# Performance work log

Hardware: AMD Instinct MI355X
Metric: run time of the kernel (lower is better)

Reference implementation:

```python
import jax, jax.numpy as jnp
import numpy as np

K = 32
D = 256


def setup_inputs() -> dict:
    key = jax.random.key(0)
    k1, k2, kW, kV, kb = jax.random.split(key, 5)
    B, L1, L2 = 16, 256, 256
    x1 = jax.random.normal(k1, (B, L1, D), dtype=jnp.float32)
    x2 = jax.random.normal(k2, (B, L2, D), dtype=jnp.float32)
    # kaiming_uniform-style init bounds
    bound_W = np.sqrt(6.0 / ((1 + 5) * D))  # fan_in = d, a=sqrt(5)
    W = jax.random.uniform(kW, (K, D, D), minval=-bound_W, maxval=bound_W, dtype=jnp.float32)
    bound_V = np.sqrt(6.0 / ((1 + 5) * 2 * D))
    V = jax.random.uniform(kV, (K, 2 * D), minval=-bound_V, maxval=bound_V, dtype=jnp.float32)
    bound_b = 1.0 / np.sqrt(2 * D)
    b = jax.random.uniform(kb, (K,), minval=-bound_b, maxval=bound_b, dtype=jnp.float32)
    return {"x1": x1, "x2": x2, "W": W, "V": V, "b": b}


def reference(x1, x2, W, V, b):
    # x1: [B,L1,d], x2: [B,L2,d], W: [k,d,d], V: [k,2d], b: [k]
    d = x1.shape[-1]
    # bilinear term: (x1 W) x2^T per output channel k -> [B,k,L1,L2]
    temp = jnp.einsum('bld,kde->bkle', x1, W)            # [B,k,L1,d]
    bilinear_out = jnp.einsum('bkle,bme->bklm', temp, x2)  # [B,k,L1,L2]
    # linear term: V @ concat(x1,x2) = V1 x1 + V2 x2, broadcast-summed
    V1, V2 = V[:, :d], V[:, d:]
    lin1 = jnp.einsum('bld,kd->bkl', x1, V1)             # [B,k,L1]
    lin2 = jnp.einsum('bmd,kd->bkm', x2, V2)             # [B,k,L2]
    linear_out = lin1[:, :, :, None] + lin2[:, :, None, :] + b[None, :, None, None]
    return jax.nn.relu(bilinear_out + linear_out)
```

## Files before the change

### kernel.cpp

```cpp
#include <hip/hip_runtime.h>
#include <hip/hip_bf16.h>

typedef unsigned short u16;
typedef __bf16 bf16x8 __attribute__((ext_vector_type(8)));
typedef float f32x4 __attribute__((ext_vector_type(4)));

#define NB 16
#define NK 32
#define ND 256
#define NL 256

__device__ __forceinline__ u16 f2bf(float f) {
    __hip_bfloat16 h = __float2bfloat16(f);
    return __builtin_bit_cast(u16, h);
}

__device__ __forceinline__ void gload_lds16(const void* g, void* l) {
    __builtin_amdgcn_global_load_lds(
        (const __attribute__((address_space(1))) unsigned int*)g,
        (__attribute__((address_space(3))) unsigned int*)l, 16, 0, 0);
}


__global__ void prep_kernel(const float* __restrict__ x1, const float* __restrict__ x2,
                            const float* __restrict__ W,
                            u16* __restrict__ x1f, u16* __restrict__ x2f, u16* __restrict__ Wf) {
    int bid = blockIdx.x;
    int tid = threadIdx.x;
    const float* src; u16* dst; long f4;
    if (bid < 1024)      { src = x1; dst = x1f; f4 = (long)bid * 256 + tid; }
    else if (bid < 2048) { src = x2; dst = x2f; f4 = (long)(bid - 1024) * 256 + tid; }
    else                 { src = W;  dst = Wf;  f4 = (long)(bid - 2048) * 256 + tid; }
    long idx = f4 << 2;
    int mat = (int)(idx >> 16);
    int r = (int)((idx >> 8) & 255);
    int c = (int)(idx & 255);
    float4 v = ((const float4*)src)[f4];
    ushort4 o;
    o.x = f2bf(v.x); o.y = f2bf(v.y); o.z = f2bf(v.z); o.w = f2bf(v.w);
    int rt = r >> 4, ct = c >> 5;
    int lane = (r & 15) | (((c >> 3) & 3) << 4);
    long off = ((long)mat << 16) + (((rt << 3) + ct) << 9) + (lane << 3) + (c & 7);
    *(ushort4*)(dst + off) = o;
}

__launch_bounds__(512, 6)
__global__ void ntn_main(const u16* __restrict__ x1f, const u16* __restrict__ x2f,
                         const u16* __restrict__ Wf,
                         const float* __restrict__ V, const float* __restrict__ bb,
                         float* __restrict__ out) {
    __shared__ __align__(16) char ldsRaw[32768];
    __shared__ float rlin[64];

    int bid = blockIdx.x;
    int xcd   = bid & 7;
    int j     = bid >> 3;
    int slot  = j >> 7;
    int inner = j & 127;
    int st    = (slot << 3) | xcd;
    int kg = st >> 2, bg = st & 3;
    int k  = (kg << 3) | (inner >> 4);
    int b  = (bg << 2) | ((inner >> 2) & 3);
    int mq = inner & 3;

    int tid  = threadIdx.x;
    int lane = tid & 63;
    int wid  = tid >> 6;
    int lrow = lane & 15;
    int j4   = (lane >> 4) << 2;

    {
        const char* src = (const char*)(x2f + ((long)b << 16) + ((long)mq << 14));
#pragma unroll
        for (int it = 0; it < 4; ++it) {
            int chunk = (it << 3) + wid;
            gload_lds16(src + (chunk << 10) + (lane << 4), ldsRaw + (chunk << 10));
        }
    }

    float bk = bb[k];
    f32x4 acc[4][2];
    const f32x4 fz = {0.f, 0.f, 0.f, 0.f};
#pragma unroll
    for (int i = 0; i < 4; ++i) { acc[i][0] = fz; acc[i][1] = fz; }

    __syncthreads();

    {
        int ml = tid >> 3;
        int et = tid & 7;
        const float* v2p = V + ((long)k << 9) + 256 + (et << 5);
        float sum = 0.f;
#pragma unroll
        for (int eg = 0; eg < 4; ++eg) {
            int lp = (ml & 15) | (eg << 4);
            bf16x8 xv = *(const bf16x8*)(ldsRaw + ((((ml >> 4) << 3) + et) << 10) + (lp << 4));
            float4 va = *(const float4*)(v2p + (eg << 3));
            float4 vb = *(const float4*)(v2p + (eg << 3) + 4);
            sum += (float)xv[0] * va.x + (float)xv[1] * va.y + (float)xv[2] * va.z + (float)xv[3] * va.w
                 + (float)xv[4] * vb.x + (float)xv[5] * vb.y + (float)xv[6] * vb.z + (float)xv[7] * vb.w;
        }
        sum += __shfl_xor(sum, 1);
        sum += __shfl_xor(sum, 2);
        sum += __shfl_xor(sum, 4);
        if ((tid & 7) == 0) rlin[ml] = sum + bk;
    }

    {
        int wrA = wid >> 1;
        int wcA = wid & 1;
        const u16* wp = Wf + ((long)k << 16);
#pragma unroll
        for (int et = 0; et < 8; ++et) {
            bf16x8 af[4], bfr[2];
#pragma unroll
            for (int lt = 0; lt < 4; ++lt)
                af[lt] = *(const bf16x8*)(wp + (((((wrA << 2) + lt) << 3) + et) << 9) + (lane << 3));
#pragma unroll
            for (int nt = 0; nt < 2; ++nt)
                bfr[nt] = *(const bf16x8*)(ldsRaw + ((((((wcA << 1) + nt) << 3) + et) << 10) + (lane << 4)));
#pragma unroll
            for (int nt = 0; nt < 2; ++nt)
#pragma unroll
                for (int lt = 0; lt < 4; ++lt)
                    acc[lt][nt] = __builtin_amdgcn_mfma_f32_16x16x32_bf16(af[lt], bfr[nt], acc[lt][nt], 0, 0, 0);
        }
    }
    __syncthreads();

    {
        int wrA = wid >> 1;
        int wcA = wid & 1;
        const float* v1base = V + ((long)k << 9);
#pragma unroll
        for (int lt = 0; lt < 4; ++lt) {
            int d0 = (wrA << 6) + (lt << 4) + j4;
            float4 v1q = *(const float4*)(v1base + d0);
#pragma unroll
            for (int nt = 0; nt < 2; ++nt) {
                int m = (wcA << 5) + (nt << 4) + lrow;
                ushort4 pk;
                pk.x = f2bf(acc[lt][nt][0] + v1q.x);
                pk.y = f2bf(acc[lt][nt][1] + v1q.y);
                pk.z = f2bf(acc[lt][nt][2] + v1q.z);
                pk.w = f2bf(acc[lt][nt][3] + v1q.w);
                *(ushort4*)(ldsRaw + (m << 9) + ((d0 << 1) ^ ((m & 7) << 4))) = pk;
            }
        }
    }
    __syncthreads();

#pragma unroll
    for (int i = 0; i < 4; ++i) { acc[i][0] = fz; acc[i][1] = fz; }

    {
        const u16* x1p = x1f + ((long)b << 16);
        int lk8 = (lane >> 4) << 3;
#pragma unroll
        for (int dt = 0; dt < 8; ++dt) {
            int d = (dt << 5) + lk8;
            bf16x8 am[4], xl[2];
#pragma unroll
            for (int mt = 0; mt < 4; ++mt) {
                int m = (mt << 4) + lrow;
                am[mt] = *(const bf16x8*)(ldsRaw + (m << 9) + ((d << 1) ^ ((m & 7) << 4)));
            }
#pragma unroll
            for (int lt = 0; lt < 2; ++lt)
                xl[lt] = *(const bf16x8*)(x1p + (((((wid << 1) + lt) << 3) + dt) << 9) + (lane << 3));
#pragma unroll
            for (int lt = 0; lt < 2; ++lt)
#pragma unroll
                for (int mt = 0; mt < 4; ++mt)
                    acc[mt][lt] = __builtin_amdgcn_mfma_f32_16x16x32_bf16(am[mt], xl[lt], acc[mt][lt], 0, 0, 0);
        }
    }
    __syncthreads();

    {
        float* outp = out + (((long)(b * NK + k)) << 16) + (mq << 6);

#pragma unroll
        for (int c = 0; c < 2; ++c) {
            if ((wid >> 2) == c) {
#pragma unroll
                for (int mt = 0; mt < 4; ++mt) {
                    int mcol = (mt << 4) + j4;
                    float4 rv = *(const float4*)(rlin + mcol);
#pragma unroll
                    for (int lt = 0; lt < 2; ++lt) {
                        int row = ((wid & 3) << 5) + (lt << 4) + lrow;
                        f32x4 v;
                        v[0] = acc[mt][lt][0] + rv.x;
                        v[1] = acc[mt][lt][1] + rv.y;
                        v[2] = acc[mt][lt][2] + rv.z;
                        v[3] = acc[mt][lt][3] + rv.w;
                        v[0] = v[0] > 0.f ? v[0] : 0.f;
                        v[1] = v[1] > 0.f ? v[1] : 0.f;
                        v[2] = v[2] > 0.f ? v[2] : 0.f;
                        v[3] = v[3] > 0.f ? v[3] : 0.f;
                        *(f32x4*)(ldsRaw + (row << 8) + ((mcol << 2) ^ ((row & 7) << 4))) = v;
                    }
                }
            }
            __syncthreads();
#pragma unroll
            for (int it = 0; it < 4; ++it) {
                int g = (it << 9) + tid;
                int row = g >> 4;
                int c4  = g & 15;
                f32x4 v = *(const f32x4*)(ldsRaw + (row << 8) + ((c4 << 4) ^ ((row & 7) << 4)));
                __builtin_nontemporal_store(v, (f32x4*)(outp + ((long)((c << 7) + row) << 8) + (c4 << 2)));
            }
            if (c == 0) __syncthreads();
        }
    }
}

extern "C" void kernel_launch(void* const* d_in, const int* in_sizes, int n_in,
                              void* d_out, int out_size, void* d_ws, size_t ws_size,
                              hipStream_t stream) {
    const float* x1 = (const float*)d_in[0];
    const float* x2 = (const float*)d_in[1];
    const float* W  = (const float*)d_in[2];
    const float* V  = (const float*)d_in[3];
    const float* bb = (const float*)d_in[4];
    float* out = (float*)d_out;

    char* ws = (char*)d_ws;
    u16*   x1f  = (u16*)(ws);
    u16*   x2f  = (u16*)(ws + (2l << 20));
    u16*   Wf   = (u16*)(ws + (4l << 20));

    hipLaunchKernelGGL(prep_kernel, dim3(4096), dim3(256), 0, stream,
                       x1, x2, W, x1f, x2f, Wf);
    hipLaunchKernelGGL(ntn_main, dim3(2048), dim3(512), 0, stream,
                       x1f, x2f, Wf, V, bb, out);
}
```

Before: 70.67 us.

## Process four output channels per block and reuse the staged x2 tile

Each block now loops over four k channels, keeping its x2 tile resident in a dedicated LDS buffer instead of reloading it per channel. The grid shrinks from 2048 to 512 blocks and the occupancy hint drops from 6 to 4. The intermediate and output-staging data move to a second LDS buffer, and the block-to-(b, mq, k) mapping is changed. The epilogue barriers now wait only on LDS counters, so the global nontemporal stores can keep draining while the next channel's GEMMs run. In exchange, far fewer blocks are in flight, which may weaken latency hiding and load balance across CUs.

```diff
diff --git a/kernel.cpp b/kernel.cpp
--- a/kernel.cpp
+++ b/kernel.cpp
@@ -19,6 +19,12 @@
     __builtin_amdgcn_global_load_lds(
         (const __attribute__((address_space(1))) unsigned int*)g,
         (__attribute__((address_space(3))) unsigned int*)l, 16, 0, 0);
+}
+
+__device__ __forceinline__ void barrier_lgkm() {
+    asm volatile("s_waitcnt lgkmcnt(0)" ::: "memory");
+    __builtin_amdgcn_s_barrier();
+    asm volatile("" ::: "memory");
 }
 
 
@@ -44,175 +50,172 @@
     *(ushort4*)(dst + off) = o;
 }
 
-__launch_bounds__(512, 6)
+__launch_bounds__(512, 4)
 __global__ void ntn_main(const u16* __restrict__ x1f, const u16* __restrict__ x2f,
                          const u16* __restrict__ Wf,
                          const float* __restrict__ V, const float* __restrict__ bb,
                          float* __restrict__ out) {
-    __shared__ __align__(16) char ldsRaw[32768];
+    __shared__ __align__(16) char ldsX2[32768];
+    __shared__ __align__(16) char ldsU[32768];
     __shared__ float rlin[64];
 
     int bid = blockIdx.x;
-    int xcd   = bid & 7;
-    int j     = bid >> 3;
-    int slot  = j >> 7;
-    int inner = j & 127;
-    int st    = (slot << 3) | xcd;
-    int kg = st >> 2, bg = st & 3;
-    int k  = (kg << 3) | (inner >> 4);
-    int b  = (bg << 2) | ((inner >> 2) & 3);
-    int mq = inner & 3;
+    int xcd = bid & 7;
+    int i   = bid >> 3;
+    int b   = (xcd << 1) | (i >> 5);
+    int mq  = (i >> 3) & 3;
+    int kg  = i & 7;
 
     int tid  = threadIdx.x;
     int lane = tid & 63;
     int wid  = tid >> 6;
     int lrow = lane & 15;
     int j4   = (lane >> 4) << 2;
+    int lk8  = (lane >> 4) << 3;
 
     {
         const char* src = (const char*)(x2f + ((long)b << 16) + ((long)mq << 14));
 #pragma unroll
         for (int it = 0; it < 4; ++it) {
             int chunk = (it << 3) + wid;
-            gload_lds16(src + (chunk << 10) + (lane << 4), ldsRaw + (chunk << 10));
-        }
-    }
-
-    float bk = bb[k];
-    f32x4 acc[4][2];
-    const f32x4 fz = {0.f, 0.f, 0.f, 0.f};
-#pragma unroll
-    for (int i = 0; i < 4; ++i) { acc[i][0] = fz; acc[i][1] = fz; }
-
-    __syncthreads();
-
-    {
-        int ml = tid >> 3;
-        int et = tid & 7;
-        const float* v2p = V + ((long)k << 9) + 256 + (et << 5);
-        float sum = 0.f;
-#pragma unroll
-        for (int eg = 0; eg < 4; ++eg) {
-            int lp = (ml & 15) | (eg << 4);
-            bf16x8 xv = *(const bf16x8*)(ldsRaw + ((((ml >> 4) << 3) + et) << 10) + (lp << 4));
-            float4 va = *(const float4*)(v2p + (eg << 3));
-            float4 vb = *(const float4*)(v2p + (eg << 3) + 4);
-            sum += (float)xv[0] * va.x + (float)xv[1] * va.y + (float)xv[2] * va.z + (float)xv[3] * va.w
-                 + (float)xv[4] * vb.x + (float)xv[5] * vb.y + (float)xv[6] * vb.z + (float)xv[7] * vb.w;
-        }
-        sum += __shfl_xor(sum, 1);
-        sum += __shfl_xor(sum, 2);
-        sum += __shfl_xor(sum, 4);
-        if ((tid & 7) == 0) rlin[ml] = sum + bk;
-    }
-
-    {
-        int wrA = wid >> 1;
-        int wcA = wid & 1;
-        const u16* wp = Wf + ((long)k << 16);
-#pragma unroll
-        for (int et = 0; et < 8; ++et) {
-            bf16x8 af[4], bfr[2];
-#pragma unroll
-            for (int lt = 0; lt < 4; ++lt)
-                af[lt] = *(const bf16x8*)(wp + (((((wrA << 2) + lt) << 3) + et) << 9) + (lane << 3));
-#pragma unroll
-            for (int nt = 0; nt < 2; ++nt)
-                bfr[nt] = *(const bf16x8*)(ldsRaw + ((((((wcA << 1) + nt) << 3) + et) << 10) + (lane << 4)));
-#pragma unroll
-            for (int nt = 0; nt < 2; ++nt)
-#pragma unroll
-                for (int lt = 0; lt < 4; ++lt)
-                    acc[lt][nt] = __builtin_amdgcn_mfma_f32_16x16x32_bf16(af[lt], bfr[nt], acc[lt][nt], 0, 0, 0);
+            gload_lds16(src + (chunk << 10) + (lane << 4), ldsX2 + (chunk << 10));
         }
     }
     __syncthreads();
 
-    {
-        int wrA = wid >> 1;
-        int wcA = wid & 1;
-        const float* v1base = V + ((long)k << 9);
-#pragma unroll
-        for (int lt = 0; lt < 4; ++lt) {
-            int d0 = (wrA << 6) + (lt << 4) + j4;
-            float4 v1q = *(const float4*)(v1base + d0);
-#pragma unroll
-            for (int nt = 0; nt < 2; ++nt) {
-                int m = (wcA << 5) + (nt << 4) + lrow;
-                ushort4 pk;
-                pk.x = f2bf(acc[lt][nt][0] + v1q.x);
-                pk.y = f2bf(acc[lt][nt][1] + v1q.y);
-                pk.z = f2bf(acc[lt][nt][2] + v1q.z);
-                pk.w = f2bf(acc[lt][nt][3] + v1q.w);
-                *(ushort4*)(ldsRaw + (m << 9) + ((d0 << 1) ^ ((m & 7) << 4))) = pk;
-            }
-        }
-    }
-    __syncthreads();
-
-#pragma unroll
-    for (int i = 0; i < 4; ++i) { acc[i][0] = fz; acc[i][1] = fz; }
-
-    {
-        const u16* x1p = x1f + ((long)b << 16);
-        int lk8 = (lane >> 4) << 3;
-#pragma unroll
-        for (int dt = 0; dt < 8; ++dt) {
-            int d = (dt << 5) + lk8;
-            bf16x8 am[4], xl[2];
-#pragma unroll
-            for (int mt = 0; mt < 4; ++mt) {
-                int m = (mt << 4) + lrow;
-                am[mt] = *(const bf16x8*)(ldsRaw + (m << 9) + ((d << 1) ^ ((m & 7) << 4)));
-            }
-#pragma unroll
-            for (int lt = 0; lt < 2; ++lt)
-                xl[lt] = *(const bf16x8*)(x1p + (((((wid << 1) + lt) << 3) + dt) << 9) + (lane << 3));
-#pragma unroll
-            for (int lt = 0; lt < 2; ++lt)
-#pragma unroll
-                for (int mt = 0; mt < 4; ++mt)
-                    acc[mt][lt] = __builtin_amdgcn_mfma_f32_16x16x32_bf16(am[mt], xl[lt], acc[mt][lt], 0, 0, 0);
-        }
-    }
-    __syncthreads();
-
-    {
-        float* outp = out + (((long)(b * NK + k)) << 16) + (mq << 6);
-
-#pragma unroll
-        for (int c = 0; c < 2; ++c) {
-            if ((wid >> 2) == c) {
+    const f32x4 fz = {0.f, 0.f, 0.f, 0.f};
+
+    for (int ki = 0; ki < 4; ++ki) {
+        int k = (kg << 2) + ki;
+
+        {
+            int ml = tid >> 3;
+            int et = tid & 7;
+            const float* v2p = V + ((long)k << 9) + 256 + (et << 5);
+            float sum = 0.f;
+#pragma unroll
+            for (int eg = 0; eg < 4; ++eg) {
+                int lp = (ml & 15) | (eg << 4);
+                bf16x8 xv = *(const bf16x8*)(ldsX2 + ((((ml >> 4) << 3) + et) << 10) + (lp << 4));
+                float4 va = *(const float4*)(v2p + (eg << 3));
+                float4 vb = *(const float4*)(v2p + (eg << 3) + 4);
+                sum += (float)xv[0] * va.x + (float)xv[1] * va.y + (float)xv[2] * va.z + (float)xv[3] * va.w
+                     + (float)xv[4] * vb.x + (float)xv[5] * vb.y + (float)xv[6] * vb.z + (float)xv[7] * vb.w;
+            }
+            sum += __shfl_xor(sum, 1);
+            sum += __shfl_xor(sum, 2);
+            sum += __shfl_xor(sum, 4);
+            if ((tid & 7) == 0) rlin[ml] = sum + bb[k];
+        }
+
+        f32x4 acc[4][2];
+#pragma unroll
+        for (int q = 0; q < 4; ++q) { acc[q][0] = fz; acc[q][1] = fz; }
+        {
+            int wrA = wid >> 1;
+            int wcA = wid & 1;
+            const u16* wp = Wf + ((long)k << 16);
+#pragma unroll
+            for (int et = 0; et < 8; ++et) {
+                bf16x8 af[4], bfr[2];
+#pragma unroll
+                for (int lt = 0; lt < 4; ++lt)
+                    af[lt] = *(const bf16x8*)(wp + (((((wrA << 2) + lt) << 3) + et) << 9) + (lane << 3));
+#pragma unroll
+                for (int nt = 0; nt < 2; ++nt)
+                    bfr[nt] = *(const bf16x8*)(ldsX2 + ((((((wcA << 1) + nt) << 3) + et) << 10) + (lane << 4)));
+#pragma unroll
+                for (int nt = 0; nt < 2; ++nt)
+#pragma unroll
+                    for (int lt = 0; lt < 4; ++lt)
+                        acc[lt][nt] = __builtin_amdgcn_mfma_f32_16x16x32_bf16(af[lt], bfr[nt], acc[lt][nt], 0, 0, 0);
+            }
+        }
+        __syncthreads();
+
+        {
+            int wrA = wid >> 1;
+            int wcA = wid & 1;
+            const float* v1base = V + ((long)k << 9);
+#pragma unroll
+            for (int lt = 0; lt < 4; ++lt) {
+                int d0 = (wrA << 6) + (lt << 4) + j4;
+                float4 v1q = *(const float4*)(v1base + d0);
+#pragma unroll
+                for (int nt = 0; nt < 2; ++nt) {
+                    int m = (wcA << 5) + (nt << 4) + lrow;
+                    ushort4 pk;
+                    pk.x = f2bf(acc[lt][nt][0] + v1q.x);
+                    pk.y = f2bf(acc[lt][nt][1] + v1q.y);
+                    pk.z = f2bf(acc[lt][nt][2] + v1q.z);
+                    pk.w = f2bf(acc[lt][nt][3] + v1q.w);
+                    *(ushort4*)(ldsU + (m << 9) + ((d0 << 1) ^ ((m & 7) << 4))) = pk;
+                }
+            }
+        }
+        __syncthreads();
+
+#pragma unroll
+        for (int q = 0; q < 4; ++q) { acc[q][0] = fz; acc[q][1] = fz; }
+        {
+            const u16* x1p = x1f + ((long)b << 16);
+#pragma unroll
+            for (int dt = 0; dt < 8; ++dt) {
+                int d = (dt << 5) + lk8;
+                bf16x8 am[4], xl[2];
 #pragma unroll
                 for (int mt = 0; mt < 4; ++mt) {
-                    int mcol = (mt << 4) + j4;
-                    float4 rv = *(const float4*)(rlin + mcol);
-#pragma unroll
-                    for (int lt = 0; lt < 2; ++lt) {
-                        int row = ((wid & 3) << 5) + (lt << 4) + lrow;
-                        f32x4 v;
-                        v[0] = acc[mt][lt][0] + rv.x;
-                        v[1] = acc[mt][lt][1] + rv.y;
-                        v[2] = acc[mt][lt][2] + rv.z;
-                        v[3] = acc[mt][lt][3] + rv.w;
-                        v[0] = v[0] > 0.f ? v[0] : 0.f;
-                        v[1] = v[1] > 0.f ? v[1] : 0.f;
-                        v[2] = v[2] > 0.f ? v[2] : 0.f;
-                        v[3] = v[3] > 0.f ? v[3] : 0.f;
-                        *(f32x4*)(ldsRaw + (row << 8) + ((mcol << 2) ^ ((row & 7) << 4))) = v;
+                    int m = (mt << 4) + lrow;
+                    am[mt] = *(const bf16x8*)(ldsU + (m << 9) + ((d << 1) ^ ((m & 7) << 4)));
+                }
+#pragma unroll
+                for (int lt = 0; lt < 2; ++lt)
+                    xl[lt] = *(const bf16x8*)(x1p + (((((wid << 1) + lt) << 3) + dt) << 9) + (lane << 3));
+#pragma unroll
+                for (int lt = 0; lt < 2; ++lt)
+#pragma unroll
+                    for (int mt = 0; mt < 4; ++mt)
+                        acc[mt][lt] = __builtin_amdgcn_mfma_f32_16x16x32_bf16(am[mt], xl[lt], acc[mt][lt], 0, 0, 0);
+            }
+        }
+        __syncthreads();
+
+        {
+            float* outp = out + (((long)(b * NK + k)) << 16) + (mq << 6);
+#pragma unroll
+            for (int c = 0; c < 2; ++c) {
+                if ((wid >> 2) == c) {
+#pragma unroll
+                    for (int mt = 0; mt < 4; ++mt) {
+                        int mcol = (mt << 4) + j4;
+                        float4 rv = *(const float4*)(rlin + mcol);
+#pragma unroll
+                        for (int lt = 0; lt < 2; ++lt) {
+                            int row = ((wid & 3) << 5) + (lt << 4) + lrow;
+                            f32x4 v;
+                            v[0] = acc[mt][lt][0] + rv.x;
+                            v[1] = acc[mt][lt][1] + rv.y;
+                            v[2] = acc[mt][lt][2] + rv.z;
+                            v[3] = acc[mt][lt][3] + rv.w;
+                            v[0] = v[0] > 0.f ? v[0] : 0.f;
+                            v[1] = v[1] > 0.f ? v[1] : 0.f;
+                            v[2] = v[2] > 0.f ? v[2] : 0.f;
+                            v[3] = v[3] > 0.f ? v[3] : 0.f;
+                            *(f32x4*)(ldsU + (row << 8) + ((mcol << 2) ^ ((row & 7) << 4))) = v;
+                        }
                     }
                 }
-            }
-            __syncthreads();
-#pragma unroll
-            for (int it = 0; it < 4; ++it) {
-                int g = (it << 9) + tid;
-                int row = g >> 4;
-                int c4  = g & 15;
-                f32x4 v = *(const f32x4*)(ldsRaw + (row << 8) + ((c4 << 4) ^ ((row & 7) << 4)));
-                __builtin_nontemporal_store(v, (f32x4*)(outp + ((long)((c << 7) + row) << 8) + (c4 << 2)));
-            }
-            if (c == 0) __syncthreads();
+                barrier_lgkm();
+#pragma unroll
+                for (int it = 0; it < 4; ++it) {
+                    int g = (it << 9) + tid;
+                    int row = g >> 4;
+                    int c4  = g & 15;
+                    f32x4 v = *(const f32x4*)(ldsU + (row << 8) + ((c4 << 4) ^ ((row & 7) << 4)));
+                    __builtin_nontemporal_store(v, (f32x4*)(outp + ((long)((c << 7) + row) << 8) + (c4 << 2)));
+                }
+                if (c == 0) barrier_lgkm();
+            }
         }
     }
 }
@@ -234,6 +237,6 @@
 
     hipLaunchKernelGGL(prep_kernel, dim3(4096), dim3(256), 0, stream,
                        x1, x2, W, x1f, x2f, Wf);
-    hipLaunchKernelGGL(ntn_main, dim3(2048), dim3(512), 0, stream,
+    hipLaunchKernelGGL(ntn_main, dim3(512), dim3(512), 0, stream,
                        x1f, x2f, Wf, V, bb, out);
 }
```

Measured after the change: 99.68 us. 1.41x slower.
